# Kernel optimization log

Hardware: AMD Instinct MI355X
Metric: run time of the kernel (lower is better)

The kernel has to match this reference:

```python
import jax, jax.numpy as jnp
import numpy as np

VOCAB_SIZE = 126
N_LABELS = VOCAB_SIZE + 2  # 128
START_IDX = N_LABELS - 2
STOP_IDX = N_LABELS - 1
NEG_INF = -10000.0


def setup_inputs() -> dict:
    key = jax.random.key(0)
    k1, k2, k3 = jax.random.split(key, 3)
    B, T = 512, 512
    logits = jax.random.normal(k1, (B, T, N_LABELS), dtype=jnp.float32)
    lens = jax.random.randint(k2, (B,), 1, T + 1, dtype=jnp.int64)
    transitions = jax.random.normal(k3, (N_LABELS, N_LABELS), dtype=jnp.float32)
    # CRF constraints from __init__: nothing transitions FROM start-as-target row,
    # nothing transitions INTO stop column (transitions[i, j] = score j -> i).
    transitions = transitions.at[START_IDX, :].set(NEG_INF)
    transitions = transitions.at[:, STOP_IDX].set(NEG_INF)
    return {"logits": logits, "lens": lens, "transitions": transitions}


def reference(logits, lens, transitions):
    """CRF forward algorithm (log partition function). Returns [B] norm."""
    B, T, n = logits.shape
    alpha0 = jnp.full((B, n), NEG_INF, dtype=logits.dtype).at[:, START_IDX].set(0.0)
    # mask[t, b] = 1 while t < lens[b] (matches c_lens > 0 per-step update)
    mask = (jnp.arange(T)[:, None] < lens[None, :]).astype(logits.dtype)  # [T, B]
    logits_t = jnp.transpose(logits, (1, 0, 2))  # [T, B, n]

    def step(alpha, inp):
        logit, m = inp  # [B, n], [B]
        # alpha_nxt[b, i] = logit[b, i] + logsumexp_j(trans[i, j] + alpha[b, j])
        alpha_nxt = jax.nn.logsumexp(transitions[None, :, :] + alpha[:, None, :], axis=2) + logit
        m = m[:, None]
        alpha = m * alpha_nxt + (1.0 - m) * alpha
        return alpha, None

    alpha, _ = jax.lax.scan(step, alpha0, (logits_t, mask))
    alpha = alpha + transitions[STOP_IDX][None, :]
    return jax.nn.logsumexp(alpha, axis=1)  # [B]
```

## Files before the change

kernel.cpp:

```cpp
#include <hip/hip_runtime.h>

#define NL 128
#define TT 512
#define NB 512
#define START_IDX 126
#define STOP_IDX 127

typedef __attribute__((ext_vector_type(8))) short bf16x8;
typedef __attribute__((ext_vector_type(4))) float f32x4;
typedef __attribute__((ext_vector_type(4))) unsigned u32x4;

__device__ __forceinline__ short f2bf(float x) {
    union { float f; unsigned u; } v; v.f = x;
    unsigned r = (v.u + 0x7FFFu + ((v.u >> 16) & 1u)) >> 16;
    return (short)r;
}

__device__ __forceinline__ unsigned cvt_pk_bf16(float lo, float hi) {
    unsigned r;
    asm("v_cvt_pk_bf16_f32 %0, %1, %2" : "=v"(r) : "v"(lo), "v"(hi));
    return r;
}

#define BAR() do {                                                            \
    asm volatile("s_waitcnt lgkmcnt(0)" ::: "memory");                        \
    __builtin_amdgcn_s_barrier();                                             \
} while (0)

#define MFMA16(A_, B_, C_) __builtin_amdgcn_mfma_f32_16x16x32_bf16(A_, B_, C_, 0, 0, 0)

#define STEP(T_, PUB_, CONS_, EU_, EB_, RS_, RD_) do {                        \
    u32x4 bo_ = {bw0, bw1, bw2, bw3};                                         \
    bf16x8 bO_ = __builtin_bit_cast(bf16x8, bo_);                             \
    bf16x8 bA_ = __builtin_bit_cast(bf16x8, bvA);                             \
    bf16x8 bB_ = __builtin_bit_cast(bf16x8, bvB);                             \
    bf16x8 bC_ = __builtin_bit_cast(bf16x8, bvC);                             \
    f32x4 a0_ = {0.f,0.f,0.f,0.f}, a1_ = {0.f,0.f,0.f,0.f};                   \
    a0_ = MFMA16(afr[0][0], bO_, a0_);             \
    a1_ = MFMA16(afr[1][0], bO_, a1_);                                        \
    if (CONS_) {                 \
        float mx_ = fmaxf(fmaxf(smax[0][c], smax[1][c]),                      \
                          fmaxf(smax[2][c], smax[3][c]));                     \
        const unsigned eb_ = (__float_as_uint(mx_) >> 23) & 0xFFu;            \
        const float sc_ = __uint_as_float(((253u - eb_) & 0xFFu) << 23);      \
        _Pragma("unroll")                                                     \
        for (int r_ = 0; r_ < 4; ++r_) {                                      \
            EU_##A[r_] *= sc_;  EU_##B[r_] *= sc_;                            \
        }                                                                     \
        if ((T_) < lenc) cbi += (int)eb_ - 126;                               \
    }                                                                         \
    { int tp_ = (T_) + 3; if (tp_ > TT - 1) tp_ = TT - 1;                     \
      const float* lp_ = lsrc + (size_t)tp_ * NL;                             \
      RD_##A = *(const f32x4*)(lp_ + eo0);                                    \
      RD_##B = *(const f32x4*)(lp_ + eo1); }                                  \
    _Pragma("unroll")               \
    for (int r_ = 0; r_ < 4; ++r_) {                                          \
        EB_##A[r_] = __expf(RS_##A[r_]);                                      \
        EB_##B[r_] = __expf(RS_##B[r_]);                                      \
    }                                                                         \
    a0_ = MFMA16(afr[0][1], bA_, a0_);                                        \
    a1_ = MFMA16(afr[1][1], bA_, a1_);                                        \
    a0_ = MFMA16(afr[0][2], bB_, a0_);                                        \
    a1_ = MFMA16(afr[1][2], bB_, a1_);                                        \
    a0_ = MFMA16(afr[0][3], bC_, a0_);                                        \
    a1_ = MFMA16(afr[1][3], bC_, a1_);                                        \
    float nv0_[4], nv1_[4];                                                   \
    _Pragma("unroll")                                                         \
    for (int r_ = 0; r_ < 4; ++r_) {                                          \
        nv0_[r_] = a0_[r_] * EU_##A[r_];                                      \
        nv1_[r_] = a1_[r_] * EU_##B[r_];                                      \
    }                                                                         \
    const bool live_ = (T_) < lenc;                                           \
    if (PUB_) {                                                               \
        float lm_ = fmaxf(fmaxf(fmaxf(nv0_[0], nv0_[1]), fmaxf(nv0_[2], nv0_[3])), \
                          fmaxf(fmaxf(nv1_[0], nv1_[1]), fmaxf(nv1_[2], nv1_[3]))); \
        lm_ = fmaxf(lm_, __shfl_xor(lm_, 16));                                \
        lm_ = fmaxf(lm_, __shfl_xor(lm_, 32));                                \
        if (g == 0) smax[w][c] = lm_;                                         \
    }                                                                         \
    { const unsigned n0_ = cvt_pk_bf16(nv0_[0], nv0_[1]);                     \
      const unsigned n1_ = cvt_pk_bf16(nv0_[2], nv0_[3]);                     \
      const unsigned n2_ = cvt_pk_bf16(nv1_[0], nv1_[1]);                     \
      const unsigned n3_ = cvt_pk_bf16(nv1_[2], nv1_[3]);                     \
      bw0 = live_ ? n0_ : bw0;  bw1 = live_ ? n1_ : bw1;                      \
      bw2 = live_ ? n2_ : bw2;  bw3 = live_ ? n3_ : bw3; }                    \
    char* nb_ = sb[((T_) + 1) & 1];                                           \
    { u32x4 wv_ = {bw0, bw1, bw2, bw3};                                       \
      *(u32x4*)(nb_ + w * 1280 + slotOff) = wv_; }                            \
    BAR();                                                                    \
    bvA = *(const u32x4*)(nb_ + kA + slotOff);                                \
    bvB = *(const u32x4*)(nb_ + kB + slotOff);                                \
    bvC = *(const u32x4*)(nb_ + kC + slotOff);                                \
} while (0)

__global__ __launch_bounds__(256)
void crf_scan(const float* __restrict__ logits,
              const int* __restrict__ lens,
              const float* __restrict__ trans,
              float* __restrict__ out)
{
    const int b0   = blockIdx.x * 16;
    const int tid  = threadIdx.x;
    const int w    = tid >> 6;
    const int lane = tid & 63;
    const int c    = lane & 15;
    const int g    = lane >> 4;

    __shared__ __align__(16) char sb[2][4 * 16 * 80];
    __shared__ float smax[4][16];

    bf16x8 afr[2][4];
    #pragma unroll
    for (int mi = 0; mi < 2; ++mi) {
        const int M = w + 4 * mi;
        const float* rowp = trans + (M * 16 + c) * NL + 4 * g;
        #pragma unroll
        for (int pos = 0; pos < 4; ++pos) {
            const int kk = (w + pos) & 3;
            f32x4 lo4 = *(const f32x4*)(rowp + kk * 16);
            f32x4 hi4 = *(const f32x4*)(rowp + (kk + 4) * 16);
            bf16x8 a;
            #pragma unroll
            for (int j = 0; j < 4; ++j) {
                a[j]     = f2bf(__expf(lo4[j]));
                a[j + 4] = f2bf(__expf(hi4[j]));
            }
            afr[mi][pos] = a;
        }
    }

    int lenc = lens[b0 + c];
    lenc = lenc < 1 ? 1 : (lenc > TT ? TT : lenc);
    int gl = lenc;
    #pragma unroll
    for (int d = 1; d < 16; d <<= 1) { int o = __shfl_xor(gl, d); gl = gl > o ? gl : o; }
    const int glen = __builtin_amdgcn_readfirstlane(gl);

    const int slotOff = c * 80 + g * 16;
    const int kA = ((w + 1) & 3) * 1280;
    const int kB = ((w + 2) & 3) * 1280;
    const int kC = ((w + 3) & 3) * 1280;

    unsigned bw0 = 0u, bw1 = 0u, bw2 = 0u,
             bw3 = (w == 3 && g == 3) ? 0x00003F80u : 0u;
    { u32x4 z = {bw0, bw1, bw2, bw3};
      *(u32x4*)(sb[0] + w * 1280 + slotOff) = z; }
    BAR();
    u32x4 bvA = *(const u32x4*)(sb[0] + kA + slotOff);
    u32x4 bvB = *(const u32x4*)(sb[0] + kB + slotOff);
    u32x4 bvC = *(const u32x4*)(sb[0] + kC + slotOff);

    const float* lsrc = logits + (size_t)(b0 + c) * TT * NL;
    const int eo0 = w * 16 + 4 * g;
    const int eo1 = (w + 4) * 16 + 4 * g;

    f32x4 R0A, R0B, R1A, R1B, R2A, R2B, R3A, R3B;
    f32x4 E0A, E0B, E1A, E1B;
    R0A = *(const f32x4*)(lsrc + eo0);            R0B = *(const f32x4*)(lsrc + eo1);
    R1A = *(const f32x4*)(lsrc + NL + eo0);       R1B = *(const f32x4*)(lsrc + NL + eo1);
    R2A = *(const f32x4*)(lsrc + 2 * NL + eo0);   R2B = *(const f32x4*)(lsrc + 2 * NL + eo1);
    #pragma unroll
    for (int r = 0; r < 4; ++r) {
        E0A[r] = __expf(R0A[r]);  E0B[r] = __expf(R0B[r]);
    }

    int cbi = 0;
    int t = 0;
    const int tmain = glen & ~3;
    for (; t < tmain; t += 4) {
        STEP(t + 0, false, false, E0, E1, R1, R3);
        STEP(t + 1, false, false, E1, E0, R2, R0);
        STEP(t + 2, true,  false, E0, E1, R3, R1);
        STEP(t + 3, false, true,  E1, E0, R0, R2);
    }
    if (t < glen) { STEP(t, false, false, E0, E1, R1, R3); ++t; }
    if (t < glen) { STEP(t, false, false, E1, E0, R2, R0); ++t; }
    if (t < glen) { STEP(t, true,  false, E0, E1, R3, R1); ++t; }

    if (w == 0) {
        float s = 0.f;
        const float* stopr = trans + STOP_IDX * NL + 4 * g;
        u32x4 grp[4];
        grp[0] = (u32x4){bw0, bw1, bw2, bw3};
        grp[1] = bvA; grp[2] = bvB; grp[3] = bvC;
        #pragma unroll
        for (int kk = 0; kk < 4; ++kk) {
            f32x4 t0 = *(const f32x4*)(stopr + kk * 16);
            f32x4 t1 = *(const f32x4*)(stopr + (kk + 4) * 16);
            #pragma unroll
            for (int i = 0; i < 2; ++i) {
                const unsigned wd = grp[kk][i];
                s += __uint_as_float(wd << 16)         * __expf(t0[2 * i]);
                s += __uint_as_float(wd & 0xFFFF0000u) * __expf(t0[2 * i + 1]);
            }
            #pragma unroll
            for (int i = 2; i < 4; ++i) {
                const unsigned wd = grp[kk][i];
                s += __uint_as_float(wd << 16)         * __expf(t1[2 * (i - 2)]);
                s += __uint_as_float(wd & 0xFFFF0000u) * __expf(t1[2 * (i - 2) + 1]);
            }
        }
        s += __shfl_xor(s, 16);
        s += __shfl_xor(s, 32);
        if (g == 0)
            out[b0 + c] = (float)cbi * 0.69314718055994531f + __logf(s);
    }
}

extern "C" void kernel_launch(void* const* d_in, const int* in_sizes, int n_in,
                              void* d_out, int out_size, void* d_ws, size_t ws_size,
                              hipStream_t stream) {
    const float* logits = (const float*)d_in[0];
    const int*   lens   = (const int*)d_in[1];
    const float* trans  = (const float*)d_in[2];
    float*       outp   = (float*)d_out;
    crf_scan<<<NB / 16, 256, 0, stream>>>(logits, lens, trans, outp);
}
```

Baseline: 154.8 us.

## Launch one block per sequence instead of sixteen sequences per block

Each block now handles a single batch sequence, so the launch grows from 32 blocks to 512 and spreads across far more compute units. Each block runs only as many steps as its own sequence length. That removes the per-column liveness select on the bf16 state, the masked rescale-exponent update, and the group max over lengths. In exchange, all 16 MFMA columns now compute the same sequence, so the tensor-core work per step is redundant. The critical path is still about 512 serial steps, set by the longest sequence, and two blocks may now share a compute unit.

```diff
diff --git a/kernel.cpp b/kernel.cpp
--- a/kernel.cpp
+++ b/kernel.cpp
@@ -39,18 +39,18 @@
     a0_ = MFMA16(afr[0][0], bO_, a0_);             \
     a1_ = MFMA16(afr[1][0], bO_, a1_);                                        \
     if (CONS_) {                 \
-        float mx_ = fmaxf(fmaxf(smax[0][c], smax[1][c]),                      \
-                          fmaxf(smax[2][c], smax[3][c]));                     \
+        float mx_ = fmaxf(fmaxf(smax[0], smax[1]),                            \
+                          fmaxf(smax[2], smax[3]));                           \
         const unsigned eb_ = (__float_as_uint(mx_) >> 23) & 0xFFu;            \
         const float sc_ = __uint_as_float(((253u - eb_) & 0xFFu) << 23);      \
         _Pragma("unroll")                                                     \
         for (int r_ = 0; r_ < 4; ++r_) {                                      \
             EU_##A[r_] *= sc_;  EU_##B[r_] *= sc_;                            \
         }                                                                     \
-        if ((T_) < lenc) cbi += (int)eb_ - 126;                               \
+        cbi += (int)eb_ - 126;                                                \
     }                                                                         \
     { int tp_ = (T_) + 3; if (tp_ > TT - 1) tp_ = TT - 1;                     \
-      const float* lp_ = lsrc + (size_t)tp_ * NL;                             \
+      const float* lp_ = lsrc + (size_t)tp_ * NL;                            \
       RD_##A = *(const f32x4*)(lp_ + eo0);                                    \
       RD_##B = *(const f32x4*)(lp_ + eo1); }                                  \
     _Pragma("unroll")               \
@@ -70,20 +70,17 @@
         nv0_[r_] = a0_[r_] * EU_##A[r_];                                      \
         nv1_[r_] = a1_[r_] * EU_##B[r_];                                      \
     }                                                                         \
-    const bool live_ = (T_) < lenc;                                           \
     if (PUB_) {                                                               \
         float lm_ = fmaxf(fmaxf(fmaxf(nv0_[0], nv0_[1]), fmaxf(nv0_[2], nv0_[3])), \
                           fmaxf(fmaxf(nv1_[0], nv1_[1]), fmaxf(nv1_[2], nv1_[3]))); \
         lm_ = fmaxf(lm_, __shfl_xor(lm_, 16));                                \
         lm_ = fmaxf(lm_, __shfl_xor(lm_, 32));                                \
-        if (g == 0) smax[w][c] = lm_;                                         \
-    }                                                                         \
-    { const unsigned n0_ = cvt_pk_bf16(nv0_[0], nv0_[1]);                     \
-      const unsigned n1_ = cvt_pk_bf16(nv0_[2], nv0_[3]);                     \
-      const unsigned n2_ = cvt_pk_bf16(nv1_[0], nv1_[1]);                     \
-      const unsigned n3_ = cvt_pk_bf16(nv1_[2], nv1_[3]);                     \
-      bw0 = live_ ? n0_ : bw0;  bw1 = live_ ? n1_ : bw1;                      \
-      bw2 = live_ ? n2_ : bw2;  bw3 = live_ ? n3_ : bw3; }                    \
+        if (lane == 0) smax[w] = lm_;                                         \
+    }                                                                         \
+    bw0 = cvt_pk_bf16(nv0_[0], nv0_[1]);                                      \
+    bw1 = cvt_pk_bf16(nv0_[2], nv0_[3]);                                      \
+    bw2 = cvt_pk_bf16(nv1_[0], nv1_[1]);                                      \
+    bw3 = cvt_pk_bf16(nv1_[2], nv1_[3]);                                      \
     char* nb_ = sb[((T_) + 1) & 1];                                           \
     { u32x4 wv_ = {bw0, bw1, bw2, bw3};                                       \
       *(u32x4*)(nb_ + w * 1280 + slotOff) = wv_; }                            \
@@ -99,7 +96,7 @@
               const float* __restrict__ trans,
               float* __restrict__ out)
 {
-    const int b0   = blockIdx.x * 16;
+    const int b0   = blockIdx.x;
     const int tid  = threadIdx.x;
     const int w    = tid >> 6;
     const int lane = tid & 63;
@@ -107,7 +104,7 @@
     const int g    = lane >> 4;
 
     __shared__ __align__(16) char sb[2][4 * 16 * 80];
-    __shared__ float smax[4][16];
+    __shared__ float smax[4];
 
     bf16x8 afr[2][4];
     #pragma unroll
@@ -129,12 +126,9 @@
         }
     }
 
-    int lenc = lens[b0 + c];
-    lenc = lenc < 1 ? 1 : (lenc > TT ? TT : lenc);
-    int gl = lenc;
-    #pragma unroll
-    for (int d = 1; d < 16; d <<= 1) { int o = __shfl_xor(gl, d); gl = gl > o ? gl : o; }
-    const int glen = __builtin_amdgcn_readfirstlane(gl);
+    int len0 = lens[b0];
+    len0 = len0 < 1 ? 1 : (len0 > TT ? TT : len0);
+    const int len = __builtin_amdgcn_readfirstlane(len0);
 
     const int slotOff = c * 80 + g * 16;
     const int kA = ((w + 1) & 3) * 1280;
@@ -150,7 +144,7 @@
     u32x4 bvB = *(const u32x4*)(sb[0] + kB + slotOff);
     u32x4 bvC = *(const u32x4*)(sb[0] + kC + slotOff);
 
-    const float* lsrc = logits + (size_t)(b0 + c) * TT * NL;
+    const float* lsrc = logits + (size_t)b0 * TT * NL;
     const int eo0 = w * 16 + 4 * g;
     const int eo1 = (w + 4) * 16 + 4 * g;
 
@@ -166,16 +160,16 @@
 
     int cbi = 0;
     int t = 0;
-    const int tmain = glen & ~3;
+    const int tmain = len & ~3;
     for (; t < tmain; t += 4) {
         STEP(t + 0, false, false, E0, E1, R1, R3);
         STEP(t + 1, false, false, E1, E0, R2, R0);
         STEP(t + 2, true,  false, E0, E1, R3, R1);
         STEP(t + 3, false, true,  E1, E0, R0, R2);
     }
-    if (t < glen) { STEP(t, false, false, E0, E1, R1, R3); ++t; }
-    if (t < glen) { STEP(t, false, false, E1, E0, R2, R0); ++t; }
-    if (t < glen) { STEP(t, true,  false, E0, E1, R3, R1); ++t; }
+    if (t < len) { STEP(t, false, false, E0, E1, R1, R3); ++t; }
+    if (t < len) { STEP(t, false, false, E1, E0, R2, R0); ++t; }
+    if (t < len) { STEP(t, true,  false, E0, E1, R3, R1); ++t; }
 
     if (w == 0) {
         float s = 0.f;
@@ -202,8 +196,8 @@
         }
         s += __shfl_xor(s, 16);
         s += __shfl_xor(s, 32);
-        if (g == 0)
-            out[b0 + c] = (float)cbi * 0.69314718055994531f + __logf(s);
+        if (lane == 0)
+            out[b0] = (float)cbi * 0.69314718055994531f + __logf(s);
     }
 }
 
@@ -214,5 +208,5 @@
     const int*   lens   = (const int*)d_in[1];
     const float* trans  = (const float*)d_in[2];
     float*       outp   = (float*)d_out;
-    crf_scan<<<NB / 16, 256, 0, stream>>>(logits, lens, trans, outp);
-}
+    crf_scan<<<NB, 256, 0, stream>>>(logits, lens, trans, outp);
+}
```

New measurement: 176.6 us. 14.1% more time.
